# Kernel optimization log

Measured on AMD Instinct MI355X. Metric: run time of the kernel, lower is better.

## Reference

```python
import jax, jax.numpy as jnp
import numpy as np

E = 1024  # embed_dim
H = 1     # num_heads (energy_W matmul forces head_dim == embed_dim)
TEMPERATURE = 1.0


def setup_inputs() -> dict:
    key = jax.random.key(0)
    ks = jax.random.split(key, 10)
    B, S = 8, 2048
    inp = {
        "query": jax.random.normal(ks[0], (B, S, E), dtype=jnp.float32),
        "key": jax.random.normal(ks[1], (B, S, E), dtype=jnp.float32),
        "value": jax.random.normal(ks[2], (B, S, E), dtype=jnp.float32),
        "mask": jnp.ones((1, 1, S, S), dtype=jnp.int32),
        # nn.Linear params (y = x @ W.T + b)
        "Wq": jax.random.normal(ks[3], (E, E), dtype=jnp.float32) * (1.0 / np.sqrt(E)),
        "bq": jnp.zeros((E,), dtype=jnp.float32),
        "Wk": jax.random.normal(ks[4], (E, E), dtype=jnp.float32) * (1.0 / np.sqrt(E)),
        "bk": jnp.zeros((E,), dtype=jnp.float32),
        "Wv": jax.random.normal(ks[5], (E, E), dtype=jnp.float32) * (1.0 / np.sqrt(E)),
        "bv": jnp.zeros((E,), dtype=jnp.float32),
        "energy_W": jax.random.normal(ks[6], (E, E), dtype=jnp.float32),
    }
    return inp


def reference(query, key, value, mask, Wq, bq, Wk, bk, Wv, bv, energy_W):
    B, S, _ = query.shape
    hd = E // H
    # projections (torch Linear: x @ W.T + b), then split heads -> [B, H, S, hd]
    q = (query @ Wq.T + bq).reshape(B, S, H, hd).transpose(0, 2, 1, 3)
    k = (key @ Wk.T + bk).reshape(B, S, H, hd).transpose(0, 2, 1, 3)
    v = (value @ Wv.T + bv).reshape(B, S, H, hd).transpose(0, 2, 1, 3)
    # bilinear energy: (q) @ (k @ W)^T   -> [B, H, Sq, Sk]
    k_t = k @ energy_W
    energy = jnp.einsum("bhqd,bhkd->bhqk", q, k_t) / TEMPERATURE
    energy = jnp.where(mask == 0, jnp.float32(-1e9), energy)
    attn_weights = jax.nn.softmax(-energy, axis=-1)
    out = jnp.einsum("bhqk,bhkd->bhqd", attn_weights, v)
    out = out.transpose(0, 2, 1, 3).reshape(B, S, E)
    return (out, attn_weights)
```

## Files before the change

kernel.cpp:

```cpp
#include <hip/hip_runtime.h>


typedef __attribute__((ext_vector_type(8))) short short8;
typedef __attribute__((ext_vector_type(4))) float f32x4;

#define E_DIM 1024
#define S_LEN 2048
#define NB 8

__device__ __forceinline__ unsigned short rne_bf(float x) {
    unsigned int u = __float_as_uint(x);
    return (unsigned short)((u + 0x7fffu + ((u >> 16) & 1u)) >> 16);
}

__device__ __forceinline__ void splitbf(float x, unsigned short& h, unsigned short& l) {
    unsigned int u = __float_as_uint(x);
    unsigned int rh = ((u + 0x7fffu + ((u >> 16) & 1u)) >> 16) << 16;
    h = (unsigned short)(rh >> 16);
    float r = x - __uint_as_float(rh);
    unsigned int v = __float_as_uint(r);
    l = (unsigned short)((v + 0x7fffu + ((v >> 16) & 1u)) >> 16);
}

__device__ __forceinline__ void lds_cp16(const void* g, void* l) {
    __builtin_amdgcn_global_load_lds(
        (const __attribute__((address_space(1))) unsigned int*)g,
        (__attribute__((address_space(3))) unsigned int*)l, 16, 0, 0);
}

__device__ __forceinline__ void wait_vm8() { asm volatile("s_waitcnt vmcnt(8)" ::: "memory"); }
__device__ __forceinline__ void wait_vm6() { asm volatile("s_waitcnt vmcnt(6)" ::: "memory"); }
__device__ __forceinline__ void wait_vm4() { asm volatile("s_waitcnt vmcnt(4)" ::: "memory"); }
__device__ __forceinline__ void wait_vm3() { asm volatile("s_waitcnt vmcnt(3)" ::: "memory"); }
__device__ __forceinline__ void wait_vm0() { asm volatile("s_waitcnt vmcnt(0)" ::: "memory"); }

__device__ __forceinline__ void swizzle_xy(int& bx, int& by) {
    const int gx = gridDim.x, gy = gridDim.y;
    const int nwg = gx * gy;
    const int w = by * gx + bx;
    if ((gx & 3) == 0 && (gy & 3) == 0 && (((gx >> 2) * (gy >> 2)) & 7) == 0) {
        const int nchx = gx >> 2;
        const int xcd = w & 7, i = w >> 3;
        const int j = i >> 4, p = i & 15;
        const int ch = xcd + 8 * j;
        const int chy = ch / nchx, chx = ch - chy * nchx;
        by = chy * 4 + (p >> 2);
        bx = chx * 4 + (p & 3);
    } else if ((nwg & 7) == 0) {
        const int cpx = nwg >> 3;
        const int sw = (w & 7) * cpx + (w >> 3);
        bx = sw % gx;
        by = sw / gx;
    }
}

template <bool DO_L>
__global__ __launch_bounds__(256) void conv_img(
    const float* __restrict__ src, unsigned short* __restrict__ h,
    unsigned short* __restrict__ l, int ld, int nkt)
{
    const int t = threadIdx.x;
    const long long tb = ((long long)blockIdx.y * nkt + blockIdx.x) * 4096;
    const float* s0 = src + (long long)blockIdx.y * 128 * ld + blockIdx.x * 32;
#pragma unroll
    for (int i = 0; i < 4; ++i) {
        const int f = i * 256 + t;
        const int r = f >> 3;
        const int c4 = (f & 7) << 2;
        const float4 v = *(const float4*)(s0 + (long long)r * ld + c4);
        const int gg = c4 >> 3;
        const int half = (c4 >> 2) & 1;
        const long long wo = tb + (long long)(gg * 128 + r) * 8 + half * 4;
        unsigned short h0, h1, h2, h3;
        if (DO_L) {
            unsigned short l0, l1, l2, l3;
            splitbf(v.x, h0, l0); splitbf(v.y, h1, l1);
            splitbf(v.z, h2, l2); splitbf(v.w, h3, l3);
            uint2 hp, lp;
            hp.x = h0 | ((unsigned)h1 << 16); hp.y = h2 | ((unsigned)h3 << 16);
            lp.x = l0 | ((unsigned)l1 << 16); lp.y = l2 | ((unsigned)l3 << 16);
            *(uint2*)(h + wo) = hp;
            *(uint2*)(l + wo) = lp;
        } else {
            h0 = rne_bf(v.x); h1 = rne_bf(v.y); h2 = rne_bf(v.z); h3 = rne_bf(v.w);
            uint2 hp;
            hp.x = h0 | ((unsigned)h1 << 16); hp.y = h2 | ((unsigned)h3 << 16);
            *(uint2*)(h + wo) = hp;
        }
    }
}

template <int NPROD>
__global__ __launch_bounds__(512, 4) void gemm_big(
    const unsigned short* __restrict__ Ah, const unsigned short* __restrict__ Al,
    const unsigned short* __restrict__ Bh, const unsigned short* __restrict__ Bl,
    float* __restrict__ C, const float* __restrict__ bias,
    int ldC, long long bsC, int nkt, int aZrb, int bZrb)
{
    __shared__ unsigned short smb[36864];

    const int t = threadIdx.x;
    const int wv = t >> 6, lane = t & 63;
    const int wr = wv >> 1, wc = wv & 1;
    const int lr = lane & 15, gq = lane >> 4;

    int bx = blockIdx.x, by = blockIdx.y;
    swizzle_xy(bx, by);

    const long long aB0 = ((long long)blockIdx.z * aZrb + 2 * by) * nkt * 4096;
    const long long aB1 = aB0 + (long long)nkt * 4096;
    const long long bB0 = ((long long)blockIdx.z * bZrb + bx) * nkt * 4096;

    auto srcptr = [&](int s, const unsigned short*& a0, const unsigned short*& a1,
                      const unsigned short*& bS) {
        int seg, kt;
        if (NPROD == 3) {
            seg = (s >= 2 * nkt) ? 2 : (s >= nkt ? 1 : 0);
            kt = s - seg * nkt;
        } else { seg = 0; kt = s; }
        const unsigned short* aBase = ((NPROD == 3 && seg == 1) ? Al : Ah);
        const unsigned short* bBase = ((NPROD == 3 && seg == 2) ? Bl : Bh);
        a0 = aBase + aB0 + (long long)kt * 4096;
        a1 = aBase + aB1 + (long long)kt * 4096;
        bS = bBase + bB0 + (long long)kt * 4096;
    };
    auto stage = [&](const unsigned short* a0, const unsigned short* a1,
                     const unsigned short* bS, int c) {
        unsigned short* dA = smb + c * 12288;
        lds_cp16(a0 + t * 8, dA + t * 8);
        lds_cp16(a1 + t * 8, dA + 4096 + t * 8);
        lds_cp16(bS + t * 8, dA + 8192 + t * 8);
    };

    f32x4 acc[4][4] = {};
    const int nsteps = NPROD * nkt;

    {
        const unsigned short *a0, *a1, *bS;
        srcptr(0, a0, a1, bS); stage(a0, a1, bS, 0);
        srcptr(1, a0, a1, bS); stage(a0, a1, bS, 1);
    }

    int cur = 0;
    for (int s = 0; s < nsteps; ++s) {
        __builtin_amdgcn_s_barrier();
        if (s + 2 < nsteps) {
            const unsigned short *a0, *a1, *bS;
            srcptr(s + 2, a0, a1, bS);
            stage(a0, a1, bS, (cur + 2) % 3);
        }
        if (s + 2 < nsteps) wait_vm6();
        else if (s + 1 < nsteps) wait_vm3();
        else wait_vm0();
        __builtin_amdgcn_s_barrier();
        __builtin_amdgcn_sched_barrier(0);

        const unsigned short* dA = smb + cur * 12288;
        const unsigned short* dB = dA + 8192;
        short8 af[4], bfr[4];
#pragma unroll
        for (int m = 0; m < 4; ++m) {
            const int R = wr * 64 + m * 16 + lr;
            af[m] = *(const short8*)(dA + (R >> 7) * 4096 + (gq * 128 + (R & 127)) * 8);
        }
#pragma unroll
        for (int n = 0; n < 4; ++n) {
            const int Cc = wc * 64 + n * 16 + lr;
            bfr[n] = *(const short8*)(dB + (gq * 128 + Cc) * 8);
        }
        __builtin_amdgcn_s_setprio(1);
#pragma unroll
        for (int m = 0; m < 4; ++m)
#pragma unroll
            for (int n = 0; n < 4; ++n)
                acc[m][n] = __builtin_amdgcn_mfma_f32_16x16x32_bf16(af[m], bfr[n], acc[m][n], 0, 0, 0);
        __builtin_amdgcn_s_setprio(0);
        cur = (cur + 1) % 3;
    }

    const int cr = (lane >> 4) << 2, cc = lane & 15;
    float* Cb = C + (long long)blockIdx.z * bsC;
#pragma unroll
    for (int m = 0; m < 4; ++m)
#pragma unroll
        for (int n = 0; n < 4; ++n) {
            const int gc = bx * 128 + wc * 64 + n * 16 + cc;
            const float badd = bias ? bias[gc] : 0.0f;
            const int gr0 = by * 256 + wr * 64 + m * 16 + cr;
#pragma unroll
            for (int i = 0; i < 4; ++i)
                Cb[(long long)(gr0 + i) * ldC + gc] = acc[m][n][i] + badd;
        }
}

template <int NPROD, int WMODE>
__global__ __launch_bounds__(256) void gemm_img(
    const unsigned short* __restrict__ Ah, const unsigned short* __restrict__ Al,
    const unsigned short* __restrict__ Bh, const unsigned short* __restrict__ Bl,
    float* __restrict__ C, const float* __restrict__ bias,
    unsigned short* __restrict__ imgH, unsigned short* __restrict__ imgL,
    int ldC, long long bsC, int nkt, int aZrb, int bZrb, int outNkt)
{
    extern __shared__ unsigned short sm[];

    const int t = threadIdx.x;
    const int wv = t >> 6, lane = t & 63;
    const int wm = (wv >> 1) << 6, wn = (wv & 1) << 6;
    const int lr = lane & 15, gq = lane >> 4;

    int bx = blockIdx.x, by = blockIdx.y;
    swizzle_xy(bx, by);

    const long long aB0 = ((long long)blockIdx.z * aZrb + by) * nkt * 4096;
    const long long bB0 = ((long long)blockIdx.z * bZrb + bx) * nkt * 4096;

    auto srcptr = [&](int s, const unsigned short*& aS, const unsigned short*& bS) {
        int seg, kt;
        if (NPROD == 3) {
            seg = (s >= 2 * nkt) ? 2 : (s >= nkt ? 1 : 0);
            kt = s - seg * nkt;
        } else { seg = 0; kt = s; }
        aS = ((NPROD == 3 && seg == 1) ? Al : Ah) + aB0 + (long long)kt * 4096;
        bS = ((NPROD == 3 && seg == 2) ? Bl : Bh) + bB0 + (long long)kt * 4096;
    };
    auto stage = [&](const unsigned short* aS, const unsigned short* bS, int c) {
        unsigned short* dA = sm + c * 8192;
        unsigned short* dB = dA + 4096;
#pragma unroll
        for (int j = 0; j < 2; ++j) {
            lds_cp16(aS + (wv * 128 + j * 64 + lane) * 8, dA + (wv * 128 + j * 64) * 8);
            lds_cp16(bS + (wv * 128 + j * 64 + lane) * 8, dB + (wv * 128 + j * 64) * 8);
        }
    };

    f32x4 acc[4][4] = {};
    const int nsteps = NPROD * nkt;

    {
        const unsigned short *aS, *bS;
        srcptr(0, aS, bS); stage(aS, bS, 0);
        srcptr(1, aS, bS); stage(aS, bS, 1);
    }

    int cur = 0;
    for (int s = 0; s < nsteps; ++s) {
        __builtin_amdgcn_s_barrier();
        if (s + 2 < nsteps) {
            const unsigned short *aS, *bS;
            srcptr(s + 2, aS, bS);
            stage(aS, bS, (cur + 2) % 3);
        }
        if (s + 2 < nsteps) wait_vm8();
        else if (s + 1 < nsteps) wait_vm4();
        else wait_vm0();
        __builtin_amdgcn_s_barrier();
        __builtin_amdgcn_sched_barrier(0);

        const unsigned short* smA = sm + cur * 8192;
        const unsigned short* smB = smA + 4096;
        short8 af[4], bfr[4];
        const unsigned short* pa = smA + (gq * 128 + wm + lr) * 8;
        const unsigned short* pb = smB + (gq * 128 + wn + lr) * 8;
#pragma unroll
        for (int m = 0; m < 4; ++m) af[m] = *(const short8*)(pa + m * 128);
#pragma unroll
        for (int n = 0; n < 4; ++n) bfr[n] = *(const short8*)(pb + n * 128);
        __builtin_amdgcn_s_setprio(1);
#pragma unroll
        for (int m = 0; m < 4; ++m)
#pragma unroll
            for (int n = 0; n < 4; ++n)
                acc[m][n] = __builtin_amdgcn_mfma_f32_16x16x32_bf16(af[m], bfr[n], acc[m][n], 0, 0, 0);
        __builtin_amdgcn_s_setprio(0);
        cur = (cur + 1) % 3;
    }

    const int cr = (lane >> 4) << 2, cc = lane & 15;
    if (WMODE == 0) {
        float* Cb = C + (long long)blockIdx.z * bsC;
#pragma unroll
        for (int m = 0; m < 4; ++m)
#pragma unroll
            for (int n = 0; n < 4; ++n) {
                const int gc = bx * 128 + wn + n * 16 + cc;
                const float badd = bias ? bias[gc] : 0.0f;
                const int gr0 = by * 128 + wm + m * 16 + cr;
#pragma unroll
                for (int i = 0; i < 4; ++i)
                    Cb[(long long)(gr0 + i) * ldC + gc] = acc[m][n][i] + badd;
            }
    } else {
        float* slab = (float*)sm;
        const int wmi = wv >> 1;
#pragma unroll
        for (int m = 0; m < 4; ++m) {
            __syncthreads();
#pragma unroll
            for (int n = 0; n < 4; ++n) {
                const int col = wn + n * 16 + cc;
                const float badd = bias ? bias[bx * 128 + col] : 0.0f;
#pragma unroll
                for (int i = 0; i < 4; ++i)
                    slab[(wmi * 16 + cr + i) * 132 + col] = acc[m][n][i] + badd;
            }
            __syncthreads();
            if (WMODE == 1) {
#pragma unroll
                for (int it = 0; it < 2; ++it) {
                    const int e = it * 256 + t;
                    const int wq = e >> 8, cg = (e >> 4) & 15, fr = e & 15;
                    const float* sp = slab + (wq * 16 + fr) * 132 + cg * 8;
                    const int rIn = wq * 64 + m * 16 + fr;
                    const int ktO = bx * 4 + (cg >> 2);
                    const int gO = cg & 3;
                    const long long base =
                        ((long long)by * outNkt + ktO) * 4096 + (gO * 128 + rIn) * 8;
                    unsigned short h[8], l[8];
#pragma unroll
                    for (int j = 0; j < 8; ++j) splitbf(sp[j], h[j], l[j]);
                    uint4 hp, lp;
                    hp.x = h[0] | ((unsigned)h[1] << 16); hp.y = h[2] | ((unsigned)h[3] << 16);
                    hp.z = h[4] | ((unsigned)h[5] << 16); hp.w = h[6] | ((unsigned)h[7] << 16);
                    lp.x = l[0] | ((unsigned)l[1] << 16); lp.y = l[2] | ((unsigned)l[3] << 16);
                    lp.z = l[4] | ((unsigned)l[5] << 16); lp.w = l[6] | ((unsigned)l[7] << 16);
                    *(uint4*)(imgH + base) = hp;
                    *(uint4*)(imgL + base) = lp;
                }
            } else {
#pragma unroll
                for (int it = 0; it < 2; ++it) {
                    const int e = it * 256 + t;
                    const int wq = e >> 8, s8 = (e >> 7) & 1, dl = e & 127;
                    const int sG = by * 128 + wq * 64 + m * 16 + s8 * 8;
                    const int z = sG >> 11, sIn = sG & 2047;
                    const int ktO = sIn >> 5, gO = (sIn >> 3) & 3;
                    const long long base =
                        ((long long)(z * 8 + bx) * 64 + ktO) * 4096 + (gO * 128 + dl) * 8;
                    unsigned short h[8];
#pragma unroll
                    for (int j = 0; j < 8; ++j)
                        h[j] = rne_bf(slab[(wq * 16 + s8 * 8 + j) * 132 + dl]);
                    uint4 hp;
                    hp.x = h[0] | ((unsigned)h[1] << 16); hp.y = h[2] | ((unsigned)h[3] << 16);
                    hp.z = h[4] | ((unsigned)h[5] << 16); hp.w = h[6] | ((unsigned)h[7] << 16);
                    *(uint4*)(imgH + base) = hp;
                }
            }
        }
    }
}

__global__ __launch_bounds__(256) void softmax_img(
    float* __restrict__ attn, const int* __restrict__ mask,
    unsigned short* __restrict__ img)
{
    const int row = blockIdx.x;
    const int q = row & (S_LEN - 1);
    const int t = threadIdx.x;
    const int lane = t & 63, wid = t >> 6;
    float* rp = attn + (long long)row * S_LEN;
    const int* mp = mask + (long long)q * S_LEN;

    const float4 e0 = *(const float4*)(rp + t * 8);
    const float4 e1 = *(const float4*)(rp + t * 8 + 4);
    const int4 ma = *(const int4*)(mp + t * 8);
    const int4 mb = *(const int4*)(mp + t * 8 + 4);
    float zv[8];
    zv[0] = ma.x ? -e0.x : 1e9f;
    zv[1] = ma.y ? -e0.y : 1e9f;
    zv[2] = ma.z ? -e0.z : 1e9f;
    zv[3] = ma.w ? -e0.w : 1e9f;
    zv[4] = mb.x ? -e1.x : 1e9f;
    zv[5] = mb.y ? -e1.y : 1e9f;
    zv[6] = mb.z ? -e1.z : 1e9f;
    zv[7] = mb.w ? -e1.w : 1e9f;
    float mx = zv[0];
#pragma unroll
    for (int j = 1; j < 8; ++j) mx = fmaxf(mx, zv[j]);
#pragma unroll
    for (int o = 32; o > 0; o >>= 1) mx = fmaxf(mx, __shfl_xor(mx, o));
    __shared__ float redm[4], reds[4];
    if (lane == 0) redm[wid] = mx;
    __syncthreads();
    mx = fmaxf(fmaxf(redm[0], redm[1]), fmaxf(redm[2], redm[3]));
    float s = 0.f;
#pragma unroll
    for (int j = 0; j < 8; ++j) { zv[j] = expf(zv[j] - mx); s += zv[j]; }
#pragma unroll
    for (int o = 32; o > 0; o >>= 1) s += __shfl_xor(s, o);
    if (lane == 0) reds[wid] = s;
    __syncthreads();
    s = reds[0] + reds[1] + reds[2] + reds[3];
    const float inv = 1.0f / s;
    float4 o0, o1;
    o0.x = zv[0] * inv; o0.y = zv[1] * inv; o0.z = zv[2] * inv; o0.w = zv[3] * inv;
    o1.x = zv[4] * inv; o1.y = zv[5] * inv; o1.z = zv[6] * inv; o1.w = zv[7] * inv;
    *(float4*)(rp + t * 8) = o0;
    *(float4*)(rp + t * 8 + 4) = o1;
    const int z = row >> 11, rb = (row >> 7) & 15;
    const int ktO = t >> 2, gO = t & 3, r = row & 127;
    const long long base = (((long long)(z * 16 + rb) * 64 + ktO) * 512 + gO * 128 + r) * 8;
    uint4 hp;
    hp.x = rne_bf(o0.x) | ((unsigned)rne_bf(o0.y) << 16);
    hp.y = rne_bf(o0.z) | ((unsigned)rne_bf(o0.w) << 16);
    hp.z = rne_bf(o1.x) | ((unsigned)rne_bf(o1.y) << 16);
    hp.w = rne_bf(o1.z) | ((unsigned)rne_bf(o1.w) << 16);
    *(uint4*)(img + base) = hp;
}

__global__ void transpose1024(const float* __restrict__ in, float* __restrict__ out)
{
    __shared__ float tile[32][33];
    const int bx = blockIdx.x << 5, by = blockIdx.y << 5;
    const int tx = threadIdx.x, ty = threadIdx.y;
#pragma unroll
    for (int i = 0; i < 4; ++i)
        tile[ty + 8 * i][tx] = in[(long long)(by + ty + 8 * i) * E_DIM + bx + tx];
    __syncthreads();
#pragma unroll
    for (int i = 0; i < 4; ++i)
        out[(long long)(bx + ty + 8 * i) * E_DIM + by + tx] = tile[tx][ty + 8 * i];
}

__global__ __launch_bounds__(256) void bias_c_kernel(
    const float* __restrict__ We, const float* __restrict__ bq, float* __restrict__ c)
{
    const int i = blockIdx.x;
    const int t = threadIdx.x;
    float s = 0.f;
    for (int d = t; d < E_DIM; d += 256) s += bq[d] * We[(long long)i * E_DIM + d];
#pragma unroll
    for (int o = 32; o > 0; o >>= 1) s += __shfl_xor(s, o);
    __shared__ float red[4];
    if ((t & 63) == 0) red[t >> 6] = s;
    __syncthreads();
    if (t == 0) c[i] = red[0] + red[1] + red[2] + red[3];
}

template <bool SPLIT, int WMODE>
__global__ __launch_bounds__(256) void gemm_split(
    const float* __restrict__ A, const float* __restrict__ B,
    float* __restrict__ C, const float* __restrict__ bias,
    int M, int N, int K,
    long long bsA, long long bsB, long long bsC)
{
    extern __shared__ unsigned short sm[];
    unsigned short* sAh = sm;
    unsigned short* sBh = sm + 5120;
    unsigned short* sAl = sm + 10240;
    unsigned short* sBl = sm + 15360;

    const int t = threadIdx.x;
    const int z = blockIdx.z;
    const float* Ab = A + (long long)z * bsA + (long long)blockIdx.y * 128 * K;
    const float* Bb = B + (long long)z * bsB + (long long)blockIdx.x * 128 * K;

    const int wv = t >> 6;
    const int lane = t & 63;
    const int wm = (wv >> 1) << 6;
    const int wn = (wv & 1) << 6;
    const int lr = lane & 15;
    const int ko = (lane >> 4) << 3;

    f32x4 acc[4][4] = {};

    for (int k0 = 0; k0 < K; k0 += 32) {
        __syncthreads();
#pragma unroll
        for (int i = 0; i < 4; ++i) {
            const int f = t + (i << 8);
            const int row = f >> 3;
            const int c4 = (f & 7) << 2;
            const float4 av = *(const float4*)(Ab + (long long)row * K + k0 + c4);
            const float4 bv = *(const float4*)(Bb + (long long)row * K + k0 + c4);
            if (SPLIT) {
                unsigned short h0, h1, h2, h3, l0, l1, l2, l3;
                splitbf(av.x, h0, l0); splitbf(av.y, h1, l1);
                splitbf(av.z, h2, l2); splitbf(av.w, h3, l3);
                uint2 hp, lp;
                hp.x = (unsigned)h0 | ((unsigned)h1 << 16);
                hp.y = (unsigned)h2 | ((unsigned)h3 << 16);
                lp.x = (unsigned)l0 | ((unsigned)l1 << 16);
                lp.y = (unsigned)l2 | ((unsigned)l3 << 16);
                *(uint2*)(sAh + row * 40 + c4) = hp;
                *(uint2*)(sAl + row * 40 + c4) = lp;
                splitbf(bv.x, h0, l0); splitbf(bv.y, h1, l1);
                splitbf(bv.z, h2, l2); splitbf(bv.w, h3, l3);
                hp.x = (unsigned)h0 | ((unsigned)h1 << 16);
                hp.y = (unsigned)h2 | ((unsigned)h3 << 16);
                lp.x = (unsigned)l0 | ((unsigned)l1 << 16);
                lp.y = (unsigned)l2 | ((unsigned)l3 << 16);
                *(uint2*)(sBh + row * 40 + c4) = hp;
                *(uint2*)(sBl + row * 40 + c4) = lp;
            } else {
                uint2 hp;
                hp.x = (unsigned)rne_bf(av.x) | ((unsigned)rne_bf(av.y) << 16);
                hp.y = (unsigned)rne_bf(av.z) | ((unsigned)rne_bf(av.w) << 16);
                *(uint2*)(sAh + row * 40 + c4) = hp;
                hp.x = (unsigned)rne_bf(bv.x) | ((unsigned)rne_bf(bv.y) << 16);
                hp.y = (unsigned)rne_bf(bv.z) | ((unsigned)rne_bf(bv.w) << 16);
                *(uint2*)(sBh + row * 40 + c4) = hp;
            }
        }
        __syncthreads();
        short8 ah[4], bh[4], al[4], bl[4];
#pragma unroll
        for (int m = 0; m < 4; ++m)
            ah[m] = *(const short8*)(sAh + (wm + m * 16 + lr) * 40 + ko);
#pragma unroll
        for (int n = 0; n < 4; ++n)
            bh[n] = *(const short8*)(sBh + (wn + n * 16 + lr) * 40 + ko);
        if (SPLIT) {
#pragma unroll
            for (int m = 0; m < 4; ++m)
                al[m] = *(const short8*)(sAl + (wm + m * 16 + lr) * 40 + ko);
#pragma unroll
            for (int n = 0; n < 4; ++n)
                bl[n] = *(const short8*)(sBl + (wn + n * 16 + lr) * 40 + ko);
        }
#pragma unroll
        for (int m = 0; m < 4; ++m) {
#pragma unroll
            for (int n = 0; n < 4; ++n) {
                acc[m][n] = __builtin_amdgcn_mfma_f32_16x16x32_bf16(ah[m], bh[n], acc[m][n], 0, 0, 0);
                if (SPLIT) {
                    acc[m][n] = __builtin_amdgcn_mfma_f32_16x16x32_bf16(ah[m], bl[n], acc[m][n], 0, 0, 0);
                    acc[m][n] = __builtin_amdgcn_mfma_f32_16x16x32_bf16(al[m], bh[n], acc[m][n], 0, 0, 0);
                }
            }
        }
    }

    const int cr = (lane >> 4) << 2;
    const int cc = lane & 15;
    float* Cb = C + (long long)z * bsC;
#pragma unroll
    for (int m = 0; m < 4; ++m) {
#pragma unroll
        for (int n = 0; n < 4; ++n) {
            const int gc = blockIdx.x * 128 + wn + n * 16 + cc;
            const float badd = bias ? bias[gc] : 0.0f;
            const int gr0 = blockIdx.y * 128 + wm + m * 16 + cr;
#pragma unroll
            for (int i = 0; i < 4; ++i) {
                const float val = acc[m][n][i] + badd;
                if (WMODE == 0) {
                    Cb[(long long)(gr0 + i) * N + gc] = val;
                } else {
                    const int r = gr0 + i;
                    Cb[(long long)(r >> 11) * ((long long)N * 2048) +
                       (long long)gc * 2048 + (r & 2047)] = val;
                }
            }
        }
    }
}

__global__ __launch_bounds__(256) void softmax_rows(
    float* __restrict__ attn, const int* __restrict__ mask)
{
    const int row = blockIdx.x;
    const int q = row & (S_LEN - 1);
    const int t = threadIdx.x;
    const int lane = t & 63, wid = t >> 6;
    float* rp = attn + (long long)row * S_LEN;
    const int* mp = mask + (long long)q * S_LEN;

    float zv[8];
    float mx = -3.4e38f;
#pragma unroll
    for (int j = 0; j < 8; ++j) {
        const int idx = t + (j << 8);
        const float e = rp[idx];
        const int mv = mp[idx];
        const float zz = (mv != 0) ? -e : 1e9f;
        zv[j] = zz;
        mx = fmaxf(mx, zz);
    }
#pragma unroll
    for (int o = 32; o > 0; o >>= 1) mx = fmaxf(mx, __shfl_xor(mx, o));
    __shared__ float redm[4], reds[4];
    if (lane == 0) redm[wid] = mx;
    __syncthreads();
    mx = fmaxf(fmaxf(redm[0], redm[1]), fmaxf(redm[2], redm[3]));

    float s = 0.f;
#pragma unroll
    for (int j = 0; j < 8; ++j) { zv[j] = expf(zv[j] - mx); s += zv[j]; }
#pragma unroll
    for (int o = 32; o > 0; o >>= 1) s += __shfl_xor(s, o);
    if (lane == 0) reds[wid] = s;
    __syncthreads();
    s = reds[0] + reds[1] + reds[2] + reds[3];
    const float inv = 1.0f / s;
#pragma unroll
    for (int j = 0; j < 8; ++j) rp[t + (j << 8)] = zv[j] * inv;
}

extern "C" void kernel_launch(void* const* d_in, const int* in_sizes, int n_in,
                              void* d_out, int out_size, void* d_ws, size_t ws_size,
                              hipStream_t stream)
{
    const float* query = (const float*)d_in[0];
    const float* key   = (const float*)d_in[1];
    const float* value = (const float*)d_in[2];
    const int*   mask  = (const int*)d_in[3];
    const float* Wq    = (const float*)d_in[4];
    const float* bq    = (const float*)d_in[5];
    const float* Wk    = (const float*)d_in[6];
    const float* bk    = (const float*)d_in[7];
    const float* Wv    = (const float*)d_in[8];
    const float* bv    = (const float*)d_in[9];
    const float* We    = (const float*)d_in[10];

    float* out  = (float*)d_out;
    float* attn = out + (long long)NB * S_LEN * E_DIM;

    const size_t oWqT  = 0;
    const size_t oCvec = oWqT + (4u << 20);
    const size_t oWqTH = oCvec + 4096;
    const size_t oWqTL = oWqTH + (2u << 20);
    const size_t oWeH  = oWqTL + (2u << 20);
    const size_t oWeL  = oWeH + (2u << 20);
    const size_t oWkH  = oWeL + (2u << 20);
    const size_t oWkL  = oWkH + (2u << 20);
    const size_t oWvH  = oWkL + (2u << 20);
    const size_t oPH   = oWvH + (2u << 20);
    const size_t oPL   = oPH + (2u << 20);
    const size_t oBig1 = oPL + (2u << 20);
    const size_t oBig2 = oBig1 + (64u << 20);
    const size_t oBig3 = oBig2 + (64u << 20);
    const size_t NEED  = oBig3 + (64u << 20);

    char* wsb = (char*)d_ws;

    if (ws_size >= NEED) {
        float* WqT  = (float*)(wsb + oWqT);
        float* cvec = (float*)(wsb + oCvec);
        unsigned short* WqTH = (unsigned short*)(wsb + oWqTH);
        unsigned short* WqTL = (unsigned short*)(wsb + oWqTL);
        unsigned short* WeH  = (unsigned short*)(wsb + oWeH);
        unsigned short* WeL  = (unsigned short*)(wsb + oWeL);
        unsigned short* WkH  = (unsigned short*)(wsb + oWkH);
        unsigned short* WkL  = (unsigned short*)(wsb + oWkL);
        unsigned short* WvH  = (unsigned short*)(wsb + oWvH);
        unsigned short* PH   = (unsigned short*)(wsb + oPH);
        unsigned short* PL   = (unsigned short*)(wsb + oPL);
        unsigned short* qryH = (unsigned short*)(wsb + oBig1);
        unsigned short* qryL = (unsigned short*)(wsb + oBig1 + (32u << 20));
        unsigned short* attnH = (unsigned short*)(wsb + oBig1);
        unsigned short* keyH = (unsigned short*)(wsb + oBig2);
        unsigned short* keyL = (unsigned short*)(wsb + oBig2 + (32u << 20));
        unsigned short* qwH  = (unsigned short*)(wsb + oBig2);
        unsigned short* qwL  = (unsigned short*)(wsb + oBig2 + (32u << 20));
        unsigned short* kH   = (unsigned short*)(wsb + oBig3);
        unsigned short* kL   = (unsigned short*)(wsb + oBig3 + (32u << 20));
        unsigned short* vTH  = (unsigned short*)(wsb + oBig3);
        unsigned short* valH = (unsigned short*)(wsb + oBig3 + (32u << 20));

        transpose1024<<<dim3(32, 32), dim3(32, 8), 0, stream>>>(Wq, WqT);
        bias_c_kernel<<<1024, 256, 0, stream>>>(We, bq, cvec);
        conv_img<true><<<dim3(32, 8), 256, 0, stream>>>(WqT, WqTH, WqTL, 1024, 32);
        conv_img<true><<<dim3(32, 8), 256, 0, stream>>>(We, WeH, WeL, 1024, 32);
        conv_img<true><<<dim3(32, 8), 256, 0, stream>>>(Wk, WkH, WkL, 1024, 32);
        conv_img<false><<<dim3(32, 8), 256, 0, stream>>>(Wv, WvH, nullptr, 1024, 32);
        conv_img<true><<<dim3(32, 128), 256, 0, stream>>>(query, qryH, qryL, 1024, 32);
        conv_img<true><<<dim3(32, 128), 256, 0, stream>>>(key, keyH, keyL, 1024, 32);

        gemm_img<3, 1><<<dim3(8, 8, 1), 256, 49152, stream>>>(
            WeH, WeL, WqTH, WqTL, nullptr, nullptr, PH, PL, 0, 0, 32, 0, 0, 32);
        gemm_img<3, 1><<<dim3(8, 128, 1), 256, 49152, stream>>>(
            keyH, keyL, WkH, WkL, nullptr, bk, kH, kL, 0, 0, 32, 0, 0, 32);
        gemm_img<3, 1><<<dim3(8, 128, 1), 256, 49152, stream>>>(
            qryH, qryL, PH, PL, nullptr, cvec, qwH, qwL, 0, 0, 32, 0, 0, 32);
        gemm_big<3><<<dim3(16, 8, NB), 512, 0, stream>>>(
            qwH, qwL, kH, kL, attn, nullptr,
            2048, (long long)S_LEN * S_LEN, 32, 16, 16);
        conv_img<false><<<dim3(32, 128), 256, 0, stream>>>(value, valH, nullptr, 1024, 32);
        gemm_img<1, 3><<<dim3(8, 128, 1), 256, 49152, stream>>>(
            valH, nullptr, WvH, nullptr, nullptr, bv, vTH, nullptr, 0, 0, 32, 0, 0, 0);
        softmax_img<<<NB * S_LEN, 256, 0, stream>>>(attn, mask, attnH);
        gemm_big<1><<<dim3(8, 8, NB), 512, 0, stream>>>(
            attnH, nullptr, vTH, nullptr, out, nullptr,
            1024, (long long)S_LEN * E_DIM, 64, 16, 8);
    } else {
        float* ws   = (float*)d_ws;
        float* WqT  = ws;
        float* P    = WqT + 1048576;
        float* cvec = P + 1048576;
        float* kbuf = cvec + 1024;
        float* qw   = kbuf + 16777216;
        float* vT   = qw + 16777216;
        const size_t need_old = (size_t)(1048576 * 2 + 1024 + 16777216 * 3) * 4;
        if (ws_size < need_old) return;

        transpose1024<<<dim3(32, 32), dim3(32, 8), 0, stream>>>(Wq, WqT);
        bias_c_kernel<<<1024, 256, 0, stream>>>(We, bq, cvec);
        gemm_split<true, 0><<<dim3(8, 8, 1), 256, 40960, stream>>>(
            We, WqT, P, nullptr, 1024, 1024, 1024, 0, 0, 0);
        gemm_split<true, 0><<<dim3(8, 128, 1), 256, 40960, stream>>>(
            key, Wk, kbuf, bk, 16384, 1024, 1024, 0, 0, 0);
        gemm_split<false, 1><<<dim3(8, 128, 1), 256, 20480, stream>>>(
            value, Wv, vT, bv, 16384, 1024, 1024, 0, 0, 0);
        gemm_split<true, 0><<<dim3(8, 128, 1), 256, 40960, stream>>>(
            query, P, qw, cvec, 16384, 1024, 1024, 0, 0, 0);
        gemm_split<true, 0><<<dim3(16, 16, NB), 256, 40960, stream>>>(
            qw, kbuf, attn, nullptr, 2048, 2048, 1024,
            (long long)S_LEN * E_DIM, (long long)S_LEN * E_DIM, (long long)S_LEN * S_LEN);
        softmax_rows<<<NB * S_LEN, 256, 0, stream>>>(attn, mask);
        gemm_split<false, 0><<<dim3(8, 16, NB), 256, 20480, stream>>>(
            attn, vT, out, nullptr, 2048, 1024, 2048,
            (long long)S_LEN * S_LEN, (long long)E_DIM * S_LEN, (long long)S_LEN * E_DIM);
    }

    (void)in_sizes; (void)n_in; (void)out_size;
}
```

Measured before the change: 797.4 us.

## Prefetch next-stage LDS fragments after MFMAs and fuse Wq transpose into conversion

Both GEMM kernels now read the next stage's A/B fragments from LDS right after issuing the current stage's MFMAs, so LDS reads overlap with matrix math instead of stalling before it. The vmcnt waits are tightened to match, and fragment loading is moved into a reusable lambda. A new conv_imgT kernel transposes Wq through shared memory while splitting it into bf16 hi/lo parts, which removes the separate transpose launch and its fp32 intermediate buffer. The tighter waits and the prefetch ordering add risk around barrier placement and buffer reuse.

```diff
diff --git a/kernel.cpp b/kernel.cpp
--- a/kernel.cpp
+++ b/kernel.cpp
@@ -28,8 +28,6 @@
         (__attribute__((address_space(3))) unsigned int*)l, 16, 0, 0);
 }
 
-__device__ __forceinline__ void wait_vm8() { asm volatile("s_waitcnt vmcnt(8)" ::: "memory"); }
-__device__ __forceinline__ void wait_vm6() { asm volatile("s_waitcnt vmcnt(6)" ::: "memory"); }
 __device__ __forceinline__ void wait_vm4() { asm volatile("s_waitcnt vmcnt(4)" ::: "memory"); }
 __device__ __forceinline__ void wait_vm3() { asm volatile("s_waitcnt vmcnt(3)" ::: "memory"); }
 __device__ __forceinline__ void wait_vm0() { asm volatile("s_waitcnt vmcnt(0)" ::: "memory"); }
@@ -90,6 +88,43 @@
     }
 }
 
+__global__ __launch_bounds__(256) void conv_imgT(
+    const float* __restrict__ src, unsigned short* __restrict__ h,
+    unsigned short* __restrict__ l, int nkt)
+{
+    __shared__ float tile[32][132];
+    const int t = threadIdx.x;
+    const int kt = blockIdx.x;
+    const int rb = blockIdx.y;
+    const float* s0 = src + (long long)kt * 32 * E_DIM + rb * 128;
+#pragma unroll
+    for (int i = 0; i < 4; ++i) {
+        const int f = i * 256 + t;
+        const int r = f >> 5;
+        const int c4 = (f & 31) << 2;
+        const float4 v = *(const float4*)(s0 + (long long)r * E_DIM + c4);
+        tile[r][c4] = v.x; tile[r][c4 + 1] = v.y;
+        tile[r][c4 + 2] = v.z; tile[r][c4 + 3] = v.w;
+    }
+    __syncthreads();
+    const long long tb = ((long long)rb * nkt + kt) * 4096;
+#pragma unroll
+    for (int i = 0; i < 2; ++i) {
+        const int c = i * 256 + t;
+        const int g = c >> 7, r = c & 127;
+        unsigned short hh[8], ll[8];
+#pragma unroll
+        for (int j = 0; j < 8; ++j) splitbf(tile[g * 8 + j][r], hh[j], ll[j]);
+        uint4 hp, lp;
+        hp.x = hh[0] | ((unsigned)hh[1] << 16); hp.y = hh[2] | ((unsigned)hh[3] << 16);
+        hp.z = hh[4] | ((unsigned)hh[5] << 16); hp.w = hh[6] | ((unsigned)hh[7] << 16);
+        lp.x = ll[0] | ((unsigned)ll[1] << 16); lp.y = ll[2] | ((unsigned)ll[3] << 16);
+        lp.z = ll[4] | ((unsigned)ll[5] << 16); lp.w = ll[6] | ((unsigned)ll[7] << 16);
+        *(uint4*)(h + tb + (long long)c * 8) = hp;
+        *(uint4*)(l + tb + (long long)c * 8) = lp;
+    }
+}
+
 template <int NPROD>
 __global__ __launch_bounds__(512, 4) void gemm_big(
     const unsigned short* __restrict__ Ah, const unsigned short* __restrict__ Al,
@@ -132,6 +167,22 @@
         lds_cp16(bS + t * 8, dA + 8192 + t * 8);
     };
 
+    short8 af[4], bfr[4];
+    auto loadFrags = [&](int c) {
+        const unsigned short* dA = smb + c * 12288;
+        const unsigned short* dB = dA + 8192;
+#pragma unroll
+        for (int m = 0; m < 4; ++m) {
+            const int R = wr * 64 + m * 16 + lr;
+            af[m] = *(const short8*)(dA + (R >> 7) * 4096 + (gq * 128 + (R & 127)) * 8);
+        }
+#pragma unroll
+        for (int n = 0; n < 4; ++n) {
+            const int Cc = wc * 64 + n * 16 + lr;
+            bfr[n] = *(const short8*)(dB + (gq * 128 + Cc) * 8);
+        }
+    };
+
     f32x4 acc[4][4] = {};
     const int nsteps = NPROD * nkt;
 
@@ -140,34 +191,23 @@
         srcptr(0, a0, a1, bS); stage(a0, a1, bS, 0);
         srcptr(1, a0, a1, bS); stage(a0, a1, bS, 1);
     }
-
-    int cur = 0;
+    wait_vm3();
+    __builtin_amdgcn_s_barrier();
+    __builtin_amdgcn_sched_barrier(0);
+    loadFrags(0);
+
     for (int s = 0; s < nsteps; ++s) {
         __builtin_amdgcn_s_barrier();
         if (s + 2 < nsteps) {
             const unsigned short *a0, *a1, *bS;
             srcptr(s + 2, a0, a1, bS);
-            stage(a0, a1, bS, (cur + 2) % 3);
-        }
-        if (s + 2 < nsteps) wait_vm6();
-        else if (s + 1 < nsteps) wait_vm3();
-        else wait_vm0();
+            stage(a0, a1, bS, (s + 2) % 3);
+            wait_vm3();
+        } else {
+            wait_vm0();
+        }
         __builtin_amdgcn_s_barrier();
         __builtin_amdgcn_sched_barrier(0);
-
-        const unsigned short* dA = smb + cur * 12288;
-        const unsigned short* dB = dA + 8192;
-        short8 af[4], bfr[4];
-#pragma unroll
-        for (int m = 0; m < 4; ++m) {
-            const int R = wr * 64 + m * 16 + lr;
-            af[m] = *(const short8*)(dA + (R >> 7) * 4096 + (gq * 128 + (R & 127)) * 8);
-        }
-#pragma unroll
-        for (int n = 0; n < 4; ++n) {
-            const int Cc = wc * 64 + n * 16 + lr;
-            bfr[n] = *(const short8*)(dB + (gq * 128 + Cc) * 8);
-        }
         __builtin_amdgcn_s_setprio(1);
 #pragma unroll
         for (int m = 0; m < 4; ++m)
@@ -175,7 +215,8 @@
             for (int n = 0; n < 4; ++n)
                 acc[m][n] = __builtin_amdgcn_mfma_f32_16x16x32_bf16(af[m], bfr[n], acc[m][n], 0, 0, 0);
         __builtin_amdgcn_s_setprio(0);
-        cur = (cur + 1) % 3;
+        if (s + 1 < nsteps) loadFrags((s + 1) % 3);
+        __builtin_amdgcn_sched_barrier(0);
     }
 
     const int cr = (lane >> 4) << 2, cc = lane & 15;
@@ -233,6 +274,18 @@
         }
     };
 
+    short8 af[4], bfr[4];
+    auto loadFrags = [&](int c) {
+        const unsigned short* smA = sm + c * 8192;
+        const unsigned short* smB = smA + 4096;
+        const unsigned short* pa = smA + (gq * 128 + wm + lr) * 8;
+        const unsigned short* pb = smB + (gq * 128 + wn + lr) * 8;
+#pragma unroll
+        for (int m = 0; m < 4; ++m) af[m] = *(const short8*)(pa + m * 128);
+#pragma unroll
+        for (int n = 0; n < 4; ++n) bfr[n] = *(const short8*)(pb + n * 128);
+    };
+
     f32x4 acc[4][4] = {};
     const int nsteps = NPROD * nkt;
 
@@ -241,30 +294,23 @@
         srcptr(0, aS, bS); stage(aS, bS, 0);
         srcptr(1, aS, bS); stage(aS, bS, 1);
     }
-
-    int cur = 0;
+    wait_vm4();
+    __builtin_amdgcn_s_barrier();
+    __builtin_amdgcn_sched_barrier(0);
+    loadFrags(0);
+
     for (int s = 0; s < nsteps; ++s) {
         __builtin_amdgcn_s_barrier();
         if (s + 2 < nsteps) {
             const unsigned short *aS, *bS;
             srcptr(s + 2, aS, bS);
-            stage(aS, bS, (cur + 2) % 3);
-        }
-        if (s + 2 < nsteps) wait_vm8();
-        else if (s + 1 < nsteps) wait_vm4();
-        else wait_vm0();
+            stage(aS, bS, (s + 2) % 3);
+            wait_vm4();
+        } else {
+            wait_vm0();
+        }
         __builtin_amdgcn_s_barrier();
         __builtin_amdgcn_sched_barrier(0);
-
-        const unsigned short* smA = sm + cur * 8192;
-        const unsigned short* smB = smA + 4096;
-        short8 af[4], bfr[4];
-        const unsigned short* pa = smA + (gq * 128 + wm + lr) * 8;
-        const unsigned short* pb = smB + (gq * 128 + wn + lr) * 8;
-#pragma unroll
-        for (int m = 0; m < 4; ++m) af[m] = *(const short8*)(pa + m * 128);
-#pragma unroll
-        for (int n = 0; n < 4; ++n) bfr[n] = *(const short8*)(pb + n * 128);
         __builtin_amdgcn_s_setprio(1);
 #pragma unroll
         for (int m = 0; m < 4; ++m)
@@ -272,7 +318,8 @@
             for (int n = 0; n < 4; ++n)
                 acc[m][n] = __builtin_amdgcn_mfma_f32_16x16x32_bf16(af[m], bfr[n], acc[m][n], 0, 0, 0);
         __builtin_amdgcn_s_setprio(0);
-        cur = (cur + 1) % 3;
+        if (s + 1 < nsteps) loadFrags((s + 1) % 3);
+        __builtin_amdgcn_sched_barrier(0);
     }
 
     const int cr = (lane >> 4) << 2, cc = lane & 15;
@@ -635,7 +682,6 @@
     char* wsb = (char*)d_ws;
 
     if (ws_size >= NEED) {
-        float* WqT  = (float*)(wsb + oWqT);
         float* cvec = (float*)(wsb + oCvec);
         unsigned short* WqTH = (unsigned short*)(wsb + oWqTH);
         unsigned short* WqTL = (unsigned short*)(wsb + oWqTL);
@@ -658,9 +704,8 @@
         unsigned short* vTH  = (unsigned short*)(wsb + oBig3);
         unsigned short* valH = (unsigned short*)(wsb + oBig3 + (32u << 20));
 
-        transpose1024<<<dim3(32, 32), dim3(32, 8), 0, stream>>>(Wq, WqT);
         bias_c_kernel<<<1024, 256, 0, stream>>>(We, bq, cvec);
-        conv_img<true><<<dim3(32, 8), 256, 0, stream>>>(WqT, WqTH, WqTL, 1024, 32);
+        conv_imgT<<<dim3(32, 8), 256, 0, stream>>>(Wq, WqTH, WqTL, 32);
         conv_img<true><<<dim3(32, 8), 256, 0, stream>>>(We, WeH, WeL, 1024, 32);
         conv_img<true><<<dim3(32, 8), 256, 0, stream>>>(Wk, WkH, WkL, 1024, 32);
         conv_img<false><<<dim3(32, 8), 256, 0, stream>>>(Wv, WvH, nullptr, 1024, 32);
```

New measurement: 813.6 us. 1.02x slower.
